# Kernel optimization log

Hardware: AMD Instinct MI355X
Metric: run time of the kernel (lower is better)

Reference implementation:

```python
import jax, jax.numpy as jnp
import numpy as np

DILATIONS = (48, 76, 96, 111, 124, 135, 144, 152)


def setup_inputs() -> dict:
    key = jax.random.key(0)
    kx, kw, kb = jax.random.split(key, 3)
    B_, C_IN, H, Wd = 8, 64, 128, 512
    C_OUT = 64
    x = jax.random.normal(kx, (B_, C_IN, H, Wd), dtype=jnp.float32)
    # stacked weights for 8 parallel branches: [branch, out_ch, in_ch, kh=1, kw=3]
    W = jax.random.normal(kw, (8, C_OUT, C_IN, 1, 3), dtype=jnp.float32) * 0.05
    B = jax.random.normal(kb, (8, C_OUT), dtype=jnp.float32) * 0.05
    return {"x": x, "W": W, "B": B}


def _dilated_conv(x, w, d):
    # 'same' padding for kernel (1,3) with dilation (1,d): pad d on each side of width
    return jax.lax.conv_general_dilated(
        x, w,
        window_strides=(1, 1),
        padding=[(0, 0), (d, d)],
        rhs_dilation=(1, d),
        dimension_numbers=("NCHW", "OIHW", "NCHW"),
    )


def reference(x, W, B):
    out = None
    for i, d in enumerate(DILATIONS):  # fixed small structural loop over branches
        y = _dilated_conv(x, W[i], d) + B[i][None, :, None, None]
        out = y if out is None else out + y
    return jax.nn.relu(out)
```

## Files before the change

kernel.cpp:

```cpp
#include <hip/hip_runtime.h>
#include <hip/hip_bf16.h>
#include <stdint.h>

typedef float  f32x4 __attribute__((ext_vector_type(4)));
typedef short  s16x8 __attribute__((ext_vector_type(8)));

#define NB    8
#define CIN   64
#define COUT  64
#define HH    128
#define WW    512
#define NTAP  17
#define PADW  152
#define XROW  816
#define BUFB  (XROW * 64)
#define HW    (HH * WW)

__global__ __launch_bounds__(256) void prep_wfrag(
        const float* __restrict__ W, const float* __restrict__ Bv,
        __hip_bfloat16* __restrict__ wf, float* __restrict__ bsum) {
    int idx = blockIdx.x * 256 + threadIdx.x;
    if (idx < NTAP * 2 * 4 * 64 * 8) {
        int j  = idx & 7;
        int l  = (idx >> 3) & 63;
        int m  = (idx >> 9) & 3;
        int pp = (idx >> 11) & 1;
        int t  = idx >> 12;
        int ci = pp * 32 + 8 * (l >> 4) + j;
        int co = 16 * m + (l & 15);
        float v;
        if (t == 0) {
            v = 0.f;
            #pragma unroll
            for (int i = 0; i < NB; ++i) v += W[((i * COUT + co) * CIN + ci) * 3 + 1];
        } else if (t <= 8) {
            v = W[(((t - 1) * COUT + co) * CIN + ci) * 3 + 0];
        } else {
            v = W[(((t - 9) * COUT + co) * CIN + ci) * 3 + 2];
        }
        wf[idx] = __float2bfloat16(v);
    }
    if (idx < COUT) {
        float s = 0.f;
        #pragma unroll
        for (int i = 0; i < NB; ++i) s += Bv[i * COUT + idx];
        bsum[idx] = s;
    }
}

static constexpr int OFFS[NTAP] = {0, -48, -76, -96, -111, -124, -135, -144, -152,
                                      48,  76,  96,  111,  124,  135,  144,  152};

#define SB __builtin_amdgcn_sched_barrier(0)

#define LOADAF(AF, T0, CNT)                                                    \
    _Pragma("unroll")                                                          \
    for (int i = 0; i < (CNT); ++i)                                            \
        _Pragma("unroll")                                                      \
        for (int m = 0; m < 4; ++m)                                            \
            AF[i][m] = *reinterpret_cast<const s16x8*>(                        \
                wbase + ((T0) + i) * 8192 + m * 1024);

#define COMPTAPS(AF, T0, CNT)                                                  \
    _Pragma("unroll")                                                          \
    for (int i = 0; i < (CNT); ++i) {                                          \
        const int t      = (T0) + i;                                           \
        const int ldsrow = rowb + OFFS[t];                                     \
        const int slot   = lhi ^ ((ldsrow >> 1) & 3);                          \
        const char* bbase = rb + ldsrow * 64 + slot * 16;                      \
        s16x8 bfr[8];                                                          \
        _Pragma("unroll")                                                      \
        for (int n = 0; n < 8; ++n)                                            \
            bfr[n] = *reinterpret_cast<const s16x8*>(bbase + n * 1024);        \
        _Pragma("unroll")                                                      \
        for (int m = 0; m < 4; ++m)                                            \
            _Pragma("unroll")                                                  \
            for (int n = 0; n < 8; ++n)                                        \
                acc[m][n] = __builtin_amdgcn_mfma_f32_16x16x32_bf16(           \
                    AF[i][m], bfr[n], acc[m][n], 0, 0, 0);                     \
    }

__global__ __launch_bounds__(256, 1) void hdc_mfma(
        const float* __restrict__ x, const __hip_bfloat16* __restrict__ wf,
        const float* __restrict__ bsum, float* __restrict__ out) {
    extern __shared__ __align__(16) char smem[];

    const int tid  = threadIdx.x;
    const int wv   = tid >> 6;
    const int lane = tid & 63;
    const int l15  = lane & 15;
    const int lhi  = lane >> 4;
    const int c    = tid >> 6;
    const int wl   = tid & 63;
    const int bh0  = blockIdx.x * 4;
    const int wlo  = wv * 128;
    const int rowb = PADW + wlo + l15;

    f32x4 acc[4][8];
    #pragma unroll
    for (int m = 0; m < 4; ++m) {
        f32x4 bi = *reinterpret_cast<const f32x4*>(bsum + 16 * m + 4 * lhi);
        #pragma unroll
        for (int n = 0; n < 8; ++n) acc[m][n] = bi;
    }

    {
        const int4 z{0, 0, 0, 0};
        #pragma unroll
        for (int bb = 0; bb < 2; ++bb) {
            int4* base = reinterpret_cast<int4*>(smem + bb * BUFB);
            for (int f = tid; f < 608; f += 256) {
                base[f] = z;
                base[2656 + f] = z;
            }
        }
    }

    float4 xv0[8], xv1[8];

    auto SLOAD = [&](int u) {
        const int r = bh0 + (u >> 1);
        const int b = r >> 7, h = r & 127;
        const float* src = x +
            (((size_t)(b * CIN + (u & 1) * 32 + c * 8) * HH + h) * WW) + wl * 4;
        #pragma unroll
        for (int j = 0; j < 8; ++j) {
            xv0[j] = *reinterpret_cast<const float4*>(src + j * HW);
            xv1[j] = *reinterpret_cast<const float4*>(src + j * HW + 256);
        }
    };
    auto SWRITE = [&](int u) {
        char* dst = smem + (u & 1) * BUFB;
        #pragma unroll
        for (int q = 0; q < 2; ++q) {
            #pragma unroll
            for (int k = 0; k < 4; ++k) {
                const int row  = PADW + wl * 4 + k + q * 256;
                const int slot = c ^ ((row >> 1) & 3);
                union { __hip_bfloat16 hs[8]; int4 iv; } pk;
                #pragma unroll
                for (int j = 0; j < 8; ++j) {
                    const float4& v = q ? xv1[j] : xv0[j];
                    pk.hs[j] = __float2bfloat16(((const float*)&v)[k]);
                }
                *reinterpret_cast<int4*>(dst + row * 64 + slot * 16) = pk.iv;
            }
        }
    };

    SLOAD(0);
    asm volatile("s_waitcnt vmcnt(0)" ::: "memory");
    SB;
    SWRITE(0);
    __syncthreads();

    for (int u = 0; u < 8; ++u) {
        const char* wbase = (const char*)wf + (u & 1) * 4096 + lane * 16;
        const char* rb    = smem + (u & 1) * BUFB;

        s16x8 af0[6][4], af1[6][4], af2[5][4];

        LOADAF(af0, 0, 6)  SB;
        COMPTAPS(af0, 0, 6) SB;
        LOADAF(af1, 6, 6)  SB;
        COMPTAPS(af1, 6, 6) SB;
        LOADAF(af2, 12, 5) SB;
        if (u < 7) SLOAD(u + 1);
        SB;
        COMPTAPS(af2, 12, 5) SB;

        if (u < 7) {
            asm volatile("s_waitcnt vmcnt(0)" ::: "memory");
            SB;
            SWRITE(u + 1);
        }

        if (u & 1) {
            const int r = bh0 + (u >> 1);
            const int b = r >> 7, h = r & 127;
            float* obase = out +
                (((size_t)b * COUT + 4 * lhi) * HH + h) * WW + wlo + l15;
            #pragma unroll
            for (int m = 0; m < 4; ++m)
                #pragma unroll
                for (int n = 0; n < 8; ++n)
                    #pragma unroll
                    for (int rr = 0; rr < 4; ++rr) {
                        float v = acc[m][n][rr];
                        obase[(size_t)(16 * m + rr) * HW + 16 * n] =
                            v > 0.f ? v : 0.f;
                    }
            #pragma unroll
            for (int m = 0; m < 4; ++m) {
                f32x4 bi = *reinterpret_cast<const f32x4*>(bsum + 16 * m + 4 * lhi);
                #pragma unroll
                for (int n = 0; n < 8; ++n) acc[m][n] = bi;
            }
        }

        asm volatile("s_waitcnt lgkmcnt(0)" ::: "memory");
        SB;
        __builtin_amdgcn_s_barrier();
    }
}

#define CI_STAGE 16

__global__ void prep_weff_fb(const float* __restrict__ W, const float* __restrict__ Bv,
                             float* __restrict__ weff, float* __restrict__ bsum) {
    int idx = blockIdx.x * 256 + threadIdx.x;
    if (idx < CIN * NTAP * COUT) {
        int co = idx & 63;
        int t  = (idx >> 6) % NTAP;
        int ci = idx / (NTAP * COUT);
        float v;
        if (t == 0) {
            v = 0.f;
            #pragma unroll
            for (int i = 0; i < NB; ++i) v += W[(((i * COUT + co) * CIN + ci) * 3) + 1];
        } else if (t <= 8) {
            v = W[((((t - 1) * COUT + co) * CIN + ci) * 3) + 0];
        } else {
            v = W[((((t - 9) * COUT + co) * CIN + ci) * 3) + 2];
        }
        weff[(ci * NTAP + t) * COUT + co] = v;
    }
    if (idx < COUT) {
        float s = 0.f;
        #pragma unroll
        for (int i = 0; i < NB; ++i) s += Bv[i * COUT + idx];
        bsum[idx] = s;
    }
}

__global__ __launch_bounds__(256, 2) void hdc_fb(
        const float* __restrict__ x, const float* __restrict__ weff,
        const float* __restrict__ bsum, float* __restrict__ out) {
    __shared__ float xsf[CI_STAGE][XROW];
    const int bh  = blockIdx.x;
    const int b   = bh >> 7;
    const int h   = bh & (HH - 1);
    const int tid = threadIdx.x;
    const int cg  = tid >> 5;
    const int wl  = tid & 31;
    float acc[8][16];
    #pragma unroll
    for (int j = 0; j < 8; ++j) {
        const float bj = bsum[cg * 8 + j];
        #pragma unroll
        for (int i = 0; i < 16; ++i) acc[j][i] = bj;
    }
    const float* xrowbase = x + ((size_t)(b * CIN) * HH + h) * WW;
    for (int s = 0; s < CIN / CI_STAGE; ++s) {
        __syncthreads();
        for (int f = tid; f < CI_STAGE * PADW; f += 256) {
            int r = f / PADW, cc = f - r * PADW;
            xsf[r][cc] = 0.f;
            xsf[r][PADW + WW + cc] = 0.f;
        }
        #pragma unroll
        for (int j = 0; j < 8; ++j) {
            int flat = j * 256 + tid;
            int r = flat >> 7, c4 = flat & 127;
            const float4 v = *reinterpret_cast<const float4*>(
                xrowbase + (size_t)(s * CI_STAGE + r) * HW + c4 * 4);
            *reinterpret_cast<float4*>(&xsf[r][PADW + c4 * 4]) = v;
        }
        __syncthreads();
        for (int r = 0; r < CI_STAGE; ++r) {
            const int ci = s * CI_STAGE + r;
            const float* wrow = weff + (size_t)(ci * NTAP) * COUT + cg * 8;
            const float* xr   = &xsf[r][PADW + wl];
            #pragma unroll
            for (int t = 0; t < NTAP; ++t) {
                const float4 w0 = *reinterpret_cast<const float4*>(wrow + t * COUT);
                const float4 w1 = *reinterpret_cast<const float4*>(wrow + t * COUT + 4);
                float xvv[16];
                #pragma unroll
                for (int i = 0; i < 16; ++i) xvv[i] = xr[OFFS[t] + 32 * i];
                const float wv[8] = {w0.x, w0.y, w0.z, w0.w, w1.x, w1.y, w1.z, w1.w};
                #pragma unroll
                for (int j = 0; j < 8; ++j)
                    #pragma unroll
                    for (int i = 0; i < 16; ++i)
                        acc[j][i] = fmaf(wv[j], xvv[i], acc[j][i]);
            }
        }
    }
    float* outbase = out + (((size_t)b * COUT + cg * 8) * HH + h) * WW + wl;
    #pragma unroll
    for (int j = 0; j < 8; ++j)
        #pragma unroll
        for (int i = 0; i < 16; ++i) {
            float v = acc[j][i];
            outbase[(size_t)j * HW + 32 * i] = v > 0.f ? v : 0.f;
        }
}


extern "C" void kernel_launch(void* const* d_in, const int* in_sizes, int n_in,
                              void* d_out, int out_size, void* d_ws, size_t ws_size,
                              hipStream_t stream) {
    const float* x  = (const float*)d_in[0];
    const float* W  = (const float*)d_in[1];
    const float* Bv = (const float*)d_in[2];
    float* out = (float*)d_out;

    const size_t need = 139264 + 256;

    if (ws_size >= need) {
        __hip_bfloat16* wf = (__hip_bfloat16*)d_ws;
        float* bsum = (float*)((char*)d_ws + 139264);
        prep_wfrag<<<272, 256, 0, stream>>>(W, Bv, wf, bsum);
        (void)hipFuncSetAttribute((const void*)hdc_mfma,
            hipFuncAttributeMaxDynamicSharedMemorySize, 2 * BUFB);
        hdc_mfma<<<256, 256, 2 * BUFB, stream>>>(x, wf, bsum, out);
    } else {
        float* weff = (float*)d_ws;
        float* bsum = weff + (size_t)CIN * NTAP * COUT;
        prep_weff_fb<<<(CIN * NTAP * COUT + 255) / 256, 256, 0, stream>>>(W, Bv, weff, bsum);
        hdc_fb<<<NB * HH, 256, 0, stream>>>(x, weff, bsum, out);
    }
}
```

Before: 84.88 us.

## Split output channels across 8 waves per block to halve per-wave accumulators

Measured after the change: 80.61 us. 5.0% less time.

```diff
diff --git a/kernel.cpp b/kernel.cpp
--- a/kernel.cpp
+++ b/kernel.cpp
@@ -57,9 +57,9 @@
     _Pragma("unroll")                                                          \
     for (int i = 0; i < (CNT); ++i)                                            \
         _Pragma("unroll")                                                      \
-        for (int m = 0; m < 4; ++m)                                            \
-            AF[i][m] = *reinterpret_cast<const s16x8*>(                        \
-                wbase + ((T0) + i) * 8192 + m * 1024);
+        for (int mm = 0; mm < 2; ++mm)                                         \
+            AF[i][mm] = *reinterpret_cast<const s16x8*>(                       \
+                wbase + ((T0) + i) * 8192 + (2 * mg + mm) * 1024);
 
 #define COMPTAPS(AF, T0, CNT)                                                  \
     _Pragma("unroll")                                                          \
@@ -73,14 +73,14 @@
         for (int n = 0; n < 8; ++n)                                            \
             bfr[n] = *reinterpret_cast<const s16x8*>(bbase + n * 1024);        \
         _Pragma("unroll")                                                      \
-        for (int m = 0; m < 4; ++m)                                            \
+        for (int mm = 0; mm < 2; ++mm)                                         \
             _Pragma("unroll")                                                  \
             for (int n = 0; n < 8; ++n)                                        \
-                acc[m][n] = __builtin_amdgcn_mfma_f32_16x16x32_bf16(           \
-                    AF[i][m], bfr[n], acc[m][n], 0, 0, 0);                     \
-    }
-
-__global__ __launch_bounds__(256, 1) void hdc_mfma(
+                acc[mm][n] = __builtin_amdgcn_mfma_f32_16x16x32_bf16(          \
+                    AF[i][mm], bfr[n], acc[mm][n], 0, 0, 0);                   \
+    }
+
+__global__ __launch_bounds__(512, 2) void hdc_mfma(
         const float* __restrict__ x, const __hip_bfloat16* __restrict__ wf,
         const float* __restrict__ bsum, float* __restrict__ out) {
     extern __shared__ __align__(16) char smem[];
@@ -90,18 +90,21 @@
     const int lane = tid & 63;
     const int l15  = lane & 15;
     const int lhi  = lane >> 4;
-    const int c    = tid >> 6;
-    const int wl   = tid & 63;
+    const int mg   = wv >> 2;
+    const int ws   = wv & 3;
+    const int c    = tid >> 7;
+    const int wl   = tid & 127;
     const int bh0  = blockIdx.x * 4;
-    const int wlo  = wv * 128;
+    const int wlo  = ws * 128;
     const int rowb = PADW + wlo + l15;
 
-    f32x4 acc[4][8];
+    f32x4 acc[2][8];
     #pragma unroll
-    for (int m = 0; m < 4; ++m) {
-        f32x4 bi = *reinterpret_cast<const f32x4*>(bsum + 16 * m + 4 * lhi);
-        #pragma unroll
-        for (int n = 0; n < 8; ++n) acc[m][n] = bi;
+    for (int mm = 0; mm < 2; ++mm) {
+        f32x4 bi = *reinterpret_cast<const f32x4*>(
+            bsum + mg * 32 + 16 * mm + 4 * lhi);
+        #pragma unroll
+        for (int n = 0; n < 8; ++n) acc[mm][n] = bi;
     }
 
     {
@@ -109,14 +112,14 @@
         #pragma unroll
         for (int bb = 0; bb < 2; ++bb) {
             int4* base = reinterpret_cast<int4*>(smem + bb * BUFB);
-            for (int f = tid; f < 608; f += 256) {
+            for (int f = tid; f < 608; f += 512) {
                 base[f] = z;
                 base[2656 + f] = z;
             }
         }
     }
 
-    float4 xv0[8], xv1[8];
+    float4 xv[8];
 
     auto SLOAD = [&](int u) {
         const int r = bh0 + (u >> 1);
@@ -124,27 +127,20 @@
         const float* src = x +
             (((size_t)(b * CIN + (u & 1) * 32 + c * 8) * HH + h) * WW) + wl * 4;
         #pragma unroll
-        for (int j = 0; j < 8; ++j) {
-            xv0[j] = *reinterpret_cast<const float4*>(src + j * HW);
-            xv1[j] = *reinterpret_cast<const float4*>(src + j * HW + 256);
-        }
+        for (int j = 0; j < 8; ++j)
+            xv[j] = *reinterpret_cast<const float4*>(src + j * HW);
     };
     auto SWRITE = [&](int u) {
         char* dst = smem + (u & 1) * BUFB;
         #pragma unroll
-        for (int q = 0; q < 2; ++q) {
-            #pragma unroll
-            for (int k = 0; k < 4; ++k) {
-                const int row  = PADW + wl * 4 + k + q * 256;
-                const int slot = c ^ ((row >> 1) & 3);
-                union { __hip_bfloat16 hs[8]; int4 iv; } pk;
-                #pragma unroll
-                for (int j = 0; j < 8; ++j) {
-                    const float4& v = q ? xv1[j] : xv0[j];
-                    pk.hs[j] = __float2bfloat16(((const float*)&v)[k]);
-                }
-                *reinterpret_cast<int4*>(dst + row * 64 + slot * 16) = pk.iv;
-            }
+        for (int k = 0; k < 4; ++k) {
+            const int row  = PADW + wl * 4 + k;
+            const int slot = c ^ ((row >> 1) & 3);
+            union { __hip_bfloat16 hs[8]; int4 iv; } pk;
+            #pragma unroll
+            for (int j = 0; j < 8; ++j)
+                pk.hs[j] = __float2bfloat16(((const float*)&xv[j])[k]);
+            *reinterpret_cast<int4*>(dst + row * 64 + slot * 16) = pk.iv;
         }
     };
 
@@ -158,44 +154,47 @@
         const char* wbase = (const char*)wf + (u & 1) * 4096 + lane * 16;
         const char* rb    = smem + (u & 1) * BUFB;
 
-        s16x8 af0[6][4], af1[6][4], af2[5][4];
-
-        LOADAF(af0, 0, 6)  SB;
-        COMPTAPS(af0, 0, 6) SB;
-        LOADAF(af1, 6, 6)  SB;
-        COMPTAPS(af1, 6, 6) SB;
-        LOADAF(af2, 12, 5) SB;
+        s16x8 af0[4][2], af1[4][2], af2[4][2], af3[5][2];
+
+        LOADAF(af0, 0, 4)  SB;
+        COMPTAPS(af0, 0, 4) SB;
+        LOADAF(af1, 4, 4)  SB;
+        COMPTAPS(af1, 4, 4) SB;
+        LOADAF(af2, 8, 4)  SB;
+        COMPTAPS(af2, 8, 4) SB;
+        LOADAF(af3, 12, 5) SB;
         if (u < 7) SLOAD(u + 1);
         SB;
-        COMPTAPS(af2, 12, 5) SB;
+        COMPTAPS(af3, 12, 5) SB;
+
+        if (u & 1) {
+            const int r = bh0 + (u >> 1);
+            const int b = r >> 7, h = r & 127;
+            float* obase = out +
+                (((size_t)b * COUT + mg * 32 + 4 * lhi) * HH + h) * WW + wlo + l15;
+            #pragma unroll
+            for (int mm = 0; mm < 2; ++mm)
+                #pragma unroll
+                for (int n = 0; n < 8; ++n)
+                    #pragma unroll
+                    for (int rr = 0; rr < 4; ++rr) {
+                        float v = acc[mm][n][rr];
+                        obase[(size_t)(16 * mm + rr) * HW + 16 * n] =
+                            v > 0.f ? v : 0.f;
+                    }
+            #pragma unroll
+            for (int mm = 0; mm < 2; ++mm) {
+                f32x4 bi = *reinterpret_cast<const f32x4*>(
+                    bsum + mg * 32 + 16 * mm + 4 * lhi);
+                #pragma unroll
+                for (int n = 0; n < 8; ++n) acc[mm][n] = bi;
+            }
+        }
 
         if (u < 7) {
             asm volatile("s_waitcnt vmcnt(0)" ::: "memory");
             SB;
             SWRITE(u + 1);
-        }
-
-        if (u & 1) {
-            const int r = bh0 + (u >> 1);
-            const int b = r >> 7, h = r & 127;
-            float* obase = out +
-                (((size_t)b * COUT + 4 * lhi) * HH + h) * WW + wlo + l15;
-            #pragma unroll
-            for (int m = 0; m < 4; ++m)
-                #pragma unroll
-                for (int n = 0; n < 8; ++n)
-                    #pragma unroll
-                    for (int rr = 0; rr < 4; ++rr) {
-                        float v = acc[m][n][rr];
-                        obase[(size_t)(16 * m + rr) * HW + 16 * n] =
-                            v > 0.f ? v : 0.f;
-                    }
-            #pragma unroll
-            for (int m = 0; m < 4; ++m) {
-                f32x4 bi = *reinterpret_cast<const f32x4*>(bsum + 16 * m + 4 * lhi);
-                #pragma unroll
-                for (int n = 0; n < 8; ++n) acc[m][n] = bi;
-            }
         }
 
         asm volatile("s_waitcnt lgkmcnt(0)" ::: "memory");
@@ -278,12 +277,12 @@
                 float xvv[16];
                 #pragma unroll
                 for (int i = 0; i < 16; ++i) xvv[i] = xr[OFFS[t] + 32 * i];
-                const float wv[8] = {w0.x, w0.y, w0.z, w0.w, w1.x, w1.y, w1.z, w1.w};
+                const float wv2[8] = {w0.x, w0.y, w0.z, w0.w, w1.x, w1.y, w1.z, w1.w};
                 #pragma unroll
                 for (int j = 0; j < 8; ++j)
                     #pragma unroll
                     for (int i = 0; i < 16; ++i)
-                        acc[j][i] = fmaf(wv[j], xvv[i], acc[j][i]);
+                        acc[j][i] = fmaf(wv2[j], xvv[i], acc[j][i]);
             }
         }
     }
@@ -314,7 +313,7 @@
         prep_wfrag<<<272, 256, 0, stream>>>(W, Bv, wf, bsum);
         (void)hipFuncSetAttribute((const void*)hdc_mfma,
             hipFuncAttributeMaxDynamicSharedMemorySize, 2 * BUFB);
-        hdc_mfma<<<256, 256, 2 * BUFB, stream>>>(x, wf, bsum, out);
+        hdc_mfma<<<256, 512, 2 * BUFB, stream>>>(x, wf, bsum, out);
     } else {
         float* weff = (float*)d_ws;
         float* bsum = weff + (size_t)CIN * NTAP * COUT;
```

## Split MFMA block into 8 waves with double-buffered weight-fragment pipeline

Applied to the files above, without the earlier changes.

After: 87.85 us. 1.04x slower.

```diff
diff --git a/kernel.cpp b/kernel.cpp
--- a/kernel.cpp
+++ b/kernel.cpp
@@ -68,19 +68,19 @@
         const int ldsrow = rowb + OFFS[t];                                     \
         const int slot   = lhi ^ ((ldsrow >> 1) & 3);                          \
         const char* bbase = rb + ldsrow * 64 + slot * 16;                      \
-        s16x8 bfr[8];                                                          \
+        s16x8 bfr[4];                                                          \
         _Pragma("unroll")                                                      \
-        for (int n = 0; n < 8; ++n)                                            \
+        for (int n = 0; n < 4; ++n)                                            \
             bfr[n] = *reinterpret_cast<const s16x8*>(bbase + n * 1024);        \
         _Pragma("unroll")                                                      \
         for (int m = 0; m < 4; ++m)                                            \
             _Pragma("unroll")                                                  \
-            for (int n = 0; n < 8; ++n)                                        \
+            for (int n = 0; n < 4; ++n)                                        \
                 acc[m][n] = __builtin_amdgcn_mfma_f32_16x16x32_bf16(           \
                     AF[i][m], bfr[n], acc[m][n], 0, 0, 0);                     \
     }
 
-__global__ __launch_bounds__(256, 1) void hdc_mfma(
+__global__ __launch_bounds__(512, 2) void hdc_mfma(
         const float* __restrict__ x, const __hip_bfloat16* __restrict__ wf,
         const float* __restrict__ bsum, float* __restrict__ out) {
     extern __shared__ __align__(16) char smem[];
@@ -90,18 +90,18 @@
     const int lane = tid & 63;
     const int l15  = lane & 15;
     const int lhi  = lane >> 4;
-    const int c    = tid >> 6;
-    const int wl   = tid & 63;
+    const int c    = tid >> 7;
+    const int wl   = tid & 127;
     const int bh0  = blockIdx.x * 4;
-    const int wlo  = wv * 128;
+    const int wlo  = wv * 64;
     const int rowb = PADW + wlo + l15;
 
-    f32x4 acc[4][8];
+    f32x4 acc[4][4];
     #pragma unroll
     for (int m = 0; m < 4; ++m) {
         f32x4 bi = *reinterpret_cast<const f32x4*>(bsum + 16 * m + 4 * lhi);
         #pragma unroll
-        for (int n = 0; n < 8; ++n) acc[m][n] = bi;
+        for (int n = 0; n < 4; ++n) acc[m][n] = bi;
     }
 
     {
@@ -109,14 +109,14 @@
         #pragma unroll
         for (int bb = 0; bb < 2; ++bb) {
             int4* base = reinterpret_cast<int4*>(smem + bb * BUFB);
-            for (int f = tid; f < 608; f += 256) {
+            for (int f = tid; f < 608; f += 512) {
                 base[f] = z;
                 base[2656 + f] = z;
             }
         }
     }
 
-    float4 xv0[8], xv1[8];
+    float4 xv[8];
 
     auto SLOAD = [&](int u) {
         const int r = bh0 + (u >> 1);
@@ -124,27 +124,20 @@
         const float* src = x +
             (((size_t)(b * CIN + (u & 1) * 32 + c * 8) * HH + h) * WW) + wl * 4;
         #pragma unroll
-        for (int j = 0; j < 8; ++j) {
-            xv0[j] = *reinterpret_cast<const float4*>(src + j * HW);
-            xv1[j] = *reinterpret_cast<const float4*>(src + j * HW + 256);
-        }
+        for (int j = 0; j < 8; ++j)
+            xv[j] = *reinterpret_cast<const float4*>(src + j * HW);
     };
     auto SWRITE = [&](int u) {
         char* dst = smem + (u & 1) * BUFB;
         #pragma unroll
-        for (int q = 0; q < 2; ++q) {
-            #pragma unroll
-            for (int k = 0; k < 4; ++k) {
-                const int row  = PADW + wl * 4 + k + q * 256;
-                const int slot = c ^ ((row >> 1) & 3);
-                union { __hip_bfloat16 hs[8]; int4 iv; } pk;
-                #pragma unroll
-                for (int j = 0; j < 8; ++j) {
-                    const float4& v = q ? xv1[j] : xv0[j];
-                    pk.hs[j] = __float2bfloat16(((const float*)&v)[k]);
-                }
-                *reinterpret_cast<int4*>(dst + row * 64 + slot * 16) = pk.iv;
-            }
+        for (int k = 0; k < 4; ++k) {
+            const int row  = PADW + wl * 4 + k;
+            const int slot = c ^ ((row >> 1) & 3);
+            union { __hip_bfloat16 hs[8]; int4 iv; } pk;
+            #pragma unroll
+            for (int j = 0; j < 8; ++j)
+                pk.hs[j] = __float2bfloat16(((const float*)&xv[j])[k]);
+            *reinterpret_cast<int4*>(dst + row * 64 + slot * 16) = pk.iv;
         }
     };
 
@@ -158,22 +151,22 @@
         const char* wbase = (const char*)wf + (u & 1) * 4096 + lane * 16;
         const char* rb    = smem + (u & 1) * BUFB;
 
-        s16x8 af0[6][4], af1[6][4], af2[5][4];
-
-        LOADAF(af0, 0, 6)  SB;
-        COMPTAPS(af0, 0, 6) SB;
-        LOADAF(af1, 6, 6)  SB;
-        COMPTAPS(af1, 6, 6) SB;
-        LOADAF(af2, 12, 5) SB;
+        s16x8 afA[3][4], afB[3][4];
+
+        LOADAF(afA, 0, 3)  SB;
+        LOADAF(afB, 3, 3)  SB;
         if (u < 7) SLOAD(u + 1);
         SB;
-        COMPTAPS(af2, 12, 5) SB;
-
-        if (u < 7) {
-            asm volatile("s_waitcnt vmcnt(0)" ::: "memory");
-            SB;
-            SWRITE(u + 1);
-        }
+        COMPTAPS(afA, 0, 3)  SB;
+        LOADAF(afA, 6, 3)  SB;
+        COMPTAPS(afB, 3, 3)  SB;
+        LOADAF(afB, 9, 3)  SB;
+        COMPTAPS(afA, 6, 3)  SB;
+        LOADAF(afA, 12, 3) SB;
+        COMPTAPS(afB, 9, 3)  SB;
+        LOADAF(afB, 15, 2) SB;
+        COMPTAPS(afA, 12, 3) SB;
+        COMPTAPS(afB, 15, 2) SB;
 
         if (u & 1) {
             const int r = bh0 + (u >> 1);
@@ -183,7 +176,7 @@
             #pragma unroll
             for (int m = 0; m < 4; ++m)
                 #pragma unroll
-                for (int n = 0; n < 8; ++n)
+                for (int n = 0; n < 4; ++n)
                     #pragma unroll
                     for (int rr = 0; rr < 4; ++rr) {
                         float v = acc[m][n][rr];
@@ -194,8 +187,14 @@
             for (int m = 0; m < 4; ++m) {
                 f32x4 bi = *reinterpret_cast<const f32x4*>(bsum + 16 * m + 4 * lhi);
                 #pragma unroll
-                for (int n = 0; n < 8; ++n) acc[m][n] = bi;
+                for (int n = 0; n < 4; ++n) acc[m][n] = bi;
             }
+        }
+
+        if (u < 7) {
+            asm volatile("s_waitcnt vmcnt(0)" ::: "memory");
+            SB;
+            SWRITE(u + 1);
         }
 
         asm volatile("s_waitcnt lgkmcnt(0)" ::: "memory");
@@ -278,12 +277,12 @@
                 float xvv[16];
                 #pragma unroll
                 for (int i = 0; i < 16; ++i) xvv[i] = xr[OFFS[t] + 32 * i];
-                const float wv[8] = {w0.x, w0.y, w0.z, w0.w, w1.x, w1.y, w1.z, w1.w};
+                const float wv2[8] = {w0.x, w0.y, w0.z, w0.w, w1.x, w1.y, w1.z, w1.w};
                 #pragma unroll
                 for (int j = 0; j < 8; ++j)
                     #pragma unroll
                     for (int i = 0; i < 16; ++i)
-                        acc[j][i] = fmaf(wv[j], xvv[i], acc[j][i]);
+                        acc[j][i] = fmaf(wv2[j], xvv[i], acc[j][i]);
             }
         }
     }
@@ -314,7 +313,7 @@
         prep_wfrag<<<272, 256, 0, stream>>>(W, Bv, wf, bsum);
         (void)hipFuncSetAttribute((const void*)hdc_mfma,
             hipFuncAttributeMaxDynamicSharedMemorySize, 2 * BUFB);
-        hdc_mfma<<<256, 256, 2 * BUFB, stream>>>(x, wf, bsum, out);
+        hdc_mfma<<<256, 512, 2 * BUFB, stream>>>(x, wf, bsum, out);
     } else {
         float* weff = (float*)d_ws;
         float* bsum = weff + (size_t)CIN * NTAP * COUT;
```

## Use one row per block with single LDS buffer for two-block occupancy

Applied to the files above, without the earlier changes.

Result: slower. 88.26 us (+4.0%).

```diff
diff --git a/kernel.cpp b/kernel.cpp
--- a/kernel.cpp
+++ b/kernel.cpp
@@ -67,7 +67,7 @@
         const int t      = (T0) + i;                                           \
         const int ldsrow = rowb + OFFS[t];                                     \
         const int slot   = lhi ^ ((ldsrow >> 1) & 3);                          \
-        const char* bbase = rb + ldsrow * 64 + slot * 16;                      \
+        const char* bbase = smem + ldsrow * 64 + slot * 16;                    \
         s16x8 bfr[8];                                                          \
         _Pragma("unroll")                                                      \
         for (int n = 0; n < 8; ++n)                                            \
@@ -80,19 +80,20 @@
                     AF[i][m], bfr[n], acc[m][n], 0, 0, 0);                     \
     }
 
-__global__ __launch_bounds__(256, 1) void hdc_mfma(
+__global__ __launch_bounds__(256, 2) void hdc_mfma(
         const float* __restrict__ x, const __hip_bfloat16* __restrict__ wf,
         const float* __restrict__ bsum, float* __restrict__ out) {
-    extern __shared__ __align__(16) char smem[];
+    __shared__ __align__(16) char smem[BUFB];
 
     const int tid  = threadIdx.x;
     const int wv   = tid >> 6;
     const int lane = tid & 63;
     const int l15  = lane & 15;
     const int lhi  = lane >> 4;
-    const int c    = tid >> 6;
+    const int c    = wv;
     const int wl   = tid & 63;
-    const int bh0  = blockIdx.x * 4;
+    const int row  = blockIdx.x;
+    const int b    = row >> 7, h = row & 127;
     const int wlo  = wv * 128;
     const int rowb = PADW + wlo + l15;
 
@@ -106,102 +107,87 @@
 
     {
         const int4 z{0, 0, 0, 0};
-        #pragma unroll
-        for (int bb = 0; bb < 2; ++bb) {
-            int4* base = reinterpret_cast<int4*>(smem + bb * BUFB);
-            for (int f = tid; f < 608; f += 256) {
-                base[f] = z;
-                base[2656 + f] = z;
+        int4* base = reinterpret_cast<int4*>(smem);
+        for (int f = tid; f < 608; f += 256) {
+            base[f] = z;
+            base[2656 + f] = z;
+        }
+    }
+
+    float4 xv[8];
+
+    auto SLOAD = [&](int p, int hf) {
+        const float* src = x +
+            (((size_t)(b * CIN + p * 32 + c * 8) * HH + h) * WW) +
+            hf * 256 + wl * 4;
+        #pragma unroll
+        for (int j = 0; j < 8; ++j)
+            xv[j] = *reinterpret_cast<const float4*>(src + j * HW);
+    };
+    auto SWRITE = [&](int hf) {
+        #pragma unroll
+        for (int k = 0; k < 4; ++k) {
+            const int r    = PADW + hf * 256 + wl * 4 + k;
+            const int slot = c ^ ((r >> 1) & 3);
+            union { __hip_bfloat16 hs[8]; int4 iv; } pk;
+            #pragma unroll
+            for (int j = 0; j < 8; ++j)
+                pk.hs[j] = __float2bfloat16(((const float*)&xv[j])[k]);
+            *reinterpret_cast<int4*>(smem + r * 64 + slot * 16) = pk.iv;
+        }
+    };
+
+    SLOAD(0, 0); SWRITE(0);
+    SLOAD(0, 1); SWRITE(1);
+    __syncthreads();
+
+    #pragma unroll
+    for (int p = 0; p < 2; ++p) {
+        const char* wbase = (const char*)wf + p * 4096 + lane * 16;
+
+        s16x8 afA[2][4], afB[2][4];
+
+        LOADAF(afA, 0, 2)    SB;
+        LOADAF(afB, 2, 2)    SB;
+        COMPTAPS(afA, 0, 2)  SB;
+        LOADAF(afA, 4, 2)    SB;
+        COMPTAPS(afB, 2, 2)  SB;
+        LOADAF(afB, 6, 2)    SB;
+        COMPTAPS(afA, 4, 2)  SB;
+        LOADAF(afA, 8, 2)    SB;
+        COMPTAPS(afB, 6, 2)  SB;
+        LOADAF(afB, 10, 2)   SB;
+        COMPTAPS(afA, 8, 2)  SB;
+        LOADAF(afA, 12, 2)   SB;
+        COMPTAPS(afB, 10, 2) SB;
+        LOADAF(afB, 14, 2)   SB;
+        COMPTAPS(afA, 12, 2) SB;
+        LOADAF(afA, 16, 1)   SB;
+        if (p == 0) SLOAD(1, 0);
+        SB;
+        COMPTAPS(afB, 14, 2) SB;
+        COMPTAPS(afA, 16, 1) SB;
+
+        __syncthreads();
+
+        if (p == 0) {
+            SWRITE(0);
+            SLOAD(1, 1);
+            SWRITE(1);
+            __syncthreads();
+        }
+    }
+
+    float* obase = out + (((size_t)b * COUT + 4 * lhi) * HH + h) * WW + wlo + l15;
+    #pragma unroll
+    for (int m = 0; m < 4; ++m)
+        #pragma unroll
+        for (int n = 0; n < 8; ++n)
+            #pragma unroll
+            for (int rr = 0; rr < 4; ++rr) {
+                float v = acc[m][n][rr];
+                obase[(size_t)(16 * m + rr) * HW + 16 * n] = v > 0.f ? v : 0.f;
             }
-        }
-    }
-
-    float4 xv0[8], xv1[8];
-
-    auto SLOAD = [&](int u) {
-        const int r = bh0 + (u >> 1);
-        const int b = r >> 7, h = r & 127;
-        const float* src = x +
-            (((size_t)(b * CIN + (u & 1) * 32 + c * 8) * HH + h) * WW) + wl * 4;
-        #pragma unroll
-        for (int j = 0; j < 8; ++j) {
-            xv0[j] = *reinterpret_cast<const float4*>(src + j * HW);
-            xv1[j] = *reinterpret_cast<const float4*>(src + j * HW + 256);
-        }
-    };
-    auto SWRITE = [&](int u) {
-        char* dst = smem + (u & 1) * BUFB;
-        #pragma unroll
-        for (int q = 0; q < 2; ++q) {
-            #pragma unroll
-            for (int k = 0; k < 4; ++k) {
-                const int row  = PADW + wl * 4 + k + q * 256;
-                const int slot = c ^ ((row >> 1) & 3);
-                union { __hip_bfloat16 hs[8]; int4 iv; } pk;
-                #pragma unroll
-                for (int j = 0; j < 8; ++j) {
-                    const float4& v = q ? xv1[j] : xv0[j];
-                    pk.hs[j] = __float2bfloat16(((const float*)&v)[k]);
-                }
-                *reinterpret_cast<int4*>(dst + row * 64 + slot * 16) = pk.iv;
-            }
-        }
-    };
-
-    SLOAD(0);
-    asm volatile("s_waitcnt vmcnt(0)" ::: "memory");
-    SB;
-    SWRITE(0);
-    __syncthreads();
-
-    for (int u = 0; u < 8; ++u) {
-        const char* wbase = (const char*)wf + (u & 1) * 4096 + lane * 16;
-        const char* rb    = smem + (u & 1) * BUFB;
-
-        s16x8 af0[6][4], af1[6][4], af2[5][4];
-
-        LOADAF(af0, 0, 6)  SB;
-        COMPTAPS(af0, 0, 6) SB;
-        LOADAF(af1, 6, 6)  SB;
-        COMPTAPS(af1, 6, 6) SB;
-        LOADAF(af2, 12, 5) SB;
-        if (u < 7) SLOAD(u + 1);
-        SB;
-        COMPTAPS(af2, 12, 5) SB;
-
-        if (u < 7) {
-            asm volatile("s_waitcnt vmcnt(0)" ::: "memory");
-            SB;
-            SWRITE(u + 1);
-        }
-
-        if (u & 1) {
-            const int r = bh0 + (u >> 1);
-            const int b = r >> 7, h = r & 127;
-            float* obase = out +
-                (((size_t)b * COUT + 4 * lhi) * HH + h) * WW + wlo + l15;
-            #pragma unroll
-            for (int m = 0; m < 4; ++m)
-                #pragma unroll
-                for (int n = 0; n < 8; ++n)
-                    #pragma unroll
-                    for (int rr = 0; rr < 4; ++rr) {
-                        float v = acc[m][n][rr];
-                        obase[(size_t)(16 * m + rr) * HW + 16 * n] =
-                            v > 0.f ? v : 0.f;
-                    }
-            #pragma unroll
-            for (int m = 0; m < 4; ++m) {
-                f32x4 bi = *reinterpret_cast<const f32x4*>(bsum + 16 * m + 4 * lhi);
-                #pragma unroll
-                for (int n = 0; n < 8; ++n) acc[m][n] = bi;
-            }
-        }
-
-        asm volatile("s_waitcnt lgkmcnt(0)" ::: "memory");
-        SB;
-        __builtin_amdgcn_s_barrier();
-    }
 }
 
 #define CI_STAGE 16
@@ -278,12 +264,12 @@
                 float xvv[16];
                 #pragma unroll
                 for (int i = 0; i < 16; ++i) xvv[i] = xr[OFFS[t] + 32 * i];
-                const float wv[8] = {w0.x, w0.y, w0.z, w0.w, w1.x, w1.y, w1.z, w1.w};
+                const float wv2[8] = {w0.x, w0.y, w0.z, w0.w, w1.x, w1.y, w1.z, w1.w};
                 #pragma unroll
                 for (int j = 0; j < 8; ++j)
                     #pragma unroll
                     for (int i = 0; i < 16; ++i)
-                        acc[j][i] = fmaf(wv[j], xvv[i], acc[j][i]);
+                        acc[j][i] = fmaf(wv2[j], xvv[i], acc[j][i]);
             }
         }
     }
@@ -312,9 +298,7 @@
         __hip_bfloat16* wf = (__hip_bfloat16*)d_ws;
         float* bsum = (float*)((char*)d_ws + 139264);
         prep_wfrag<<<272, 256, 0, stream>>>(W, Bv, wf, bsum);
-        (void)hipFuncSetAttribute((const void*)hdc_mfma,
-            hipFuncAttributeMaxDynamicSharedMemorySize, 2 * BUFB);
-        hdc_mfma<<<256, 256, 2 * BUFB, stream>>>(x, wf, bsum, out);
+        hdc_mfma<<<1024, 256, 0, stream>>>(x, wf, bsum, out);
     } else {
         float* weff = (float*)d_ws;
         float* bsum = weff + (size_t)CIN * NTAP * COUT;
```
